# Performance work log

Hardware: AMD Instinct MI355X
Metric: run time of the kernel (lower is better)

## Reference

```python
import jax, jax.numpy as jnp
import numpy as np

K = 4
G = 64
IN_DIM = 256
OUT_DIM = 256
BATCH = 512
T0, T1 = -1.0, 1.0


def setup_inputs() -> dict:
    key = jax.random.key(0)
    kx, kw = jax.random.split(key)
    x = jax.random.uniform(kx, (BATCH, IN_DIM), jnp.float32, T0, T1)
    # xavier_normal_ on [G+K, in, out]: std = sqrt(2 / (fan_in + fan_out)) with fan over last two dims
    std = (2.0 / (IN_DIM + OUT_DIM)) ** 0.5
    w = jax.random.normal(kw, (G + K, IN_DIM, OUT_DIM), jnp.float32) * std
    # knot vector: k-1 repeats of t0, linspace(t0,t1,G+1), k-1 repeats of t1
    t = jnp.concatenate([
        jnp.full((K - 1,), T0, jnp.float32),
        jnp.linspace(T0, T1, G + 1, dtype=jnp.float32),
        jnp.full((K - 1,), T1, jnp.float32),
    ])
    return {"x": x, "w": w, "t": t, "k": K}


def _basis(x, t, k):
    """Cox-de Boor: the k nonzero order-k B-spline basis values at each x.
    Returns (idx, N): idx [..., k] basis indices i-k+1..i, N [..., k] values."""
    n_t = t.shape[0]
    # interval i with t[i] <= x < t[i+1], clipped to the valid span
    i = jnp.clip(jnp.searchsorted(t, x, side='right') - 1, k - 1, n_t - k - 1)
    N = jnp.ones(x.shape + (1,), x.dtype)
    for p in range(1, k):  # static small loop (k=4)
        jj = jnp.arange(1, p + 1)
        left = x[..., None] - t[i[..., None] + 1 - jj]   # [..., p]
        right = t[i[..., None] + jj] - x[..., None]      # [..., p]
        saved = jnp.zeros_like(x)
        vals = []
        for r in range(p):
            d = right[..., r] + left[..., p - 1 - r]      # t[i+r+1] - t[i+r+1-p]
            temp = N[..., r] / d
            vals.append(saved + right[..., r] * temp)
            saved = left[..., p - 1 - r] * temp
        vals.append(saved)
        N = jnp.stack(vals, -1)
    idx = i[..., None] - (k - 1) + jnp.arange(k)
    return idx, N


def reference(x, w, t, k):
    in_dim = x.shape[1]
    n_rows = w.shape[0]
    idx, y1 = _basis(x, t, k)                             # [B,in,k], [B,in,k]
    # last row of w (index -1 == n_rows-1) weights the SiLU residual term
    idx_full = jnp.concatenate(
        [idx, jnp.full(idx.shape[:-1] + (1,), n_rows - 1, idx.dtype)], -1)  # [B,in,k+1]
    silu = x * jax.nn.sigmoid(x)
    y2 = jnp.concatenate([y1, silu[..., None]], -1)       # [B,in,k+1]
    # gather local spline coefficients: w2[b,c,j,o] = w[idx_full[b,c,j], c, o]
    w2 = w[idx_full, jnp.arange(in_dim)[None, :, None], :]  # [B,in,k+1,out]
    return jnp.einsum('bcjo,bcj->bo', w2, y2)             # [B,out]
```

## Files before the change

kernel.cpp:

```cpp
#include <hip/hip_runtime.h>
#include <math.h>
#include <stdint.h>

#define IN_DIM  256
#define OUT_DIM 256
#define NROWS   68
#define NT      71
#define BATCH   512
#define W_ELEMS (NROWS * IN_DIM * OUT_DIM)
#define PART_FLOATS (8 * BATCH * OUT_DIM)

__device__ __forceinline__ uint32_t bf16_rne(float f) {
  uint32_t u = __builtin_bit_cast(uint32_t, f);
  return (u + 0x7fffu + ((u >> 16) & 1u)) >> 16;
}

__global__ __launch_bounds__(256) void cvt_kernel(const float* __restrict__ w,
                                                  uint32_t* __restrict__ wb) {
  const int base = (blockIdx.x * 256 + threadIdx.x) * 8;
  const float4 a = *(const float4*)(w + base);
  const float4 b = *(const float4*)(w + base + 4);
  uint4 o;
  o.x = bf16_rne(a.x) | (bf16_rne(a.y) << 16);
  o.y = bf16_rne(a.z) | (bf16_rne(a.w) << 16);
  o.z = bf16_rne(b.x) | (bf16_rne(b.y) << 16);
  o.w = bf16_rne(b.z) | (bf16_rne(b.w) << 16);
  *(uint4*)(wb + base / 2) = o;
}

__device__ __forceinline__ void fma8(const uint4 q, const float y, float* acc) {
  acc[0] += y * __builtin_bit_cast(float, q.x << 16);
  acc[1] += y * __builtin_bit_cast(float, q.x & 0xffff0000u);
  acc[2] += y * __builtin_bit_cast(float, q.y << 16);
  acc[3] += y * __builtin_bit_cast(float, q.y & 0xffff0000u);
  acc[4] += y * __builtin_bit_cast(float, q.z << 16);
  acc[5] += y * __builtin_bit_cast(float, q.z & 0xffff0000u);
  acc[6] += y * __builtin_bit_cast(float, q.w << 16);
  acc[7] += y * __builtin_bit_cast(float, q.w & 0xffff0000u);
}

__global__ __launch_bounds__(256) void kan_gather_kernel(
    const float* __restrict__ x, const uint4* __restrict__ wp,
    const float* __restrict__ t, float* __restrict__ part) {
  __shared__ float  lt[NT];
  __shared__ float4 nA[32][8];
  __shared__ float  sA[32][8];
  __shared__ int    bA[32][8];
  __shared__ float  red[4][2048];

  const int tid = threadIdx.x;
  const unsigned bid = blockIdx.x;
  const int cchunk = bid & 7;
  const int bgroup = bid >> 3;

  if (tid < NT) lt[tid] = t[tid];
  __syncthreads();

  {
    const int bb = tid >> 5;
    const int cl = tid & 31;
    const float xv = x[(size_t)(bgroup * 8 + bb) * IN_DIM + cchunk * 32 + cl];
    int i = 3 + (int)floorf((xv + 1.0f) * 32.0f);
    i = i < 3 ? 3 : (i > 66 ? 66 : i);
    while (i > 3 && xv < lt[i]) --i;
    while (i < 66 && xv >= lt[i + 1]) ++i;

    float N0 = 1.f, N1 = 0.f, N2 = 0.f, N3 = 0.f;
    {
      const float l1 = xv - lt[i];
      const float r1 = lt[i + 1] - xv;
      const float tp = N0 / (r1 + l1);
      N1 = l1 * tp; N0 = r1 * tp;
    }
    {
      const float l1 = xv - lt[i];
      const float l2 = xv - lt[i - 1];
      const float r1 = lt[i + 1] - xv;
      const float r2 = lt[i + 2] - xv;
      float saved = 0.f;
      const float tp0 = N0 / (r1 + l2);
      const float n0 = saved + r1 * tp0; saved = l2 * tp0;
      const float tp1 = N1 / (r2 + l1);
      const float n1 = saved + r2 * tp1; saved = l1 * tp1;
      N0 = n0; N1 = n1; N2 = saved;
    }
    {
      const float l1 = xv - lt[i];
      const float l2 = xv - lt[i - 1];
      const float l3 = xv - lt[i - 2];
      const float r1 = lt[i + 1] - xv;
      const float r2 = lt[i + 2] - xv;
      const float r3 = lt[i + 3] - xv;
      float saved = 0.f;
      const float tp0 = N0 / (r1 + l3);
      const float n0 = saved + r1 * tp0; saved = l3 * tp0;
      const float tp1 = N1 / (r2 + l2);
      const float n1 = saved + r2 * tp1; saved = l2 * tp1;
      const float tp2 = N2 / (r3 + l1);
      const float n2 = saved + r3 * tp2; saved = l1 * tp2;
      N0 = n0; N1 = n1; N2 = n2; N3 = saved;
    }
    nA[cl][bb] = make_float4(N0, N1, N2, N3);
    sA[cl][bb] = xv / (1.0f + expf(-xv));
    bA[cl][bb] = i - 3;
  }
  __syncthreads();

  const int wv   = tid >> 6;
  const int lane = tid & 63;
  const int half = lane >> 5;
  const int ol   = lane & 31;

  float acc[8][8];
  #pragma unroll
  for (int b = 0; b < 8; ++b) {
    #pragma unroll
    for (int j = 0; j < 8; ++j) acc[b][j] = 0.f;
  }

  for (int pp = 0; pp < 4; ++pp) {
    const int cl = wv * 8 + pp * 2 + half;
    const uint32_t cbase = (uint32_t)((cchunk * 32 + cl) * 32 + ol);
    const uint4 q4 = wp[cbase + 67u * 8192u];
    #pragma unroll
    for (int b = 0; b < 8; ++b) {
      const float4 yv = nA[cl][b];
      const float  ys = sA[cl][b];
      const uint32_t rb = cbase + ((uint32_t)bA[cl][b] << 13);
      const uint4 q0 = wp[rb];
      const uint4 q1 = wp[rb +  8192u];
      const uint4 q2 = wp[rb + 16384u];
      const uint4 q3 = wp[rb + 24576u];
      fma8(q0, yv.x, acc[b]);
      fma8(q1, yv.y, acc[b]);
      fma8(q2, yv.z, acc[b]);
      fma8(q3, yv.w, acc[b]);
      fma8(q4, ys,   acc[b]);
    }
  }

  #pragma unroll
  for (int b = 0; b < 8; ++b) {
    #pragma unroll
    for (int j = 0; j < 8; ++j)
      acc[b][j] += __shfl_xor(acc[b][j], 32, 64);
  }

  if (half == 0) {
    #pragma unroll
    for (int b = 0; b < 8; ++b) {
      #pragma unroll
      for (int j = 0; j < 8; ++j)
        red[wv][b * 256 + ol * 8 + j] = acc[b][j];
    }
  }
  __syncthreads();

  {
    const int b  = tid >> 5;
    const int oo = tid & 31;
    float4 s0 = make_float4(0.f, 0.f, 0.f, 0.f);
    float4 s1 = make_float4(0.f, 0.f, 0.f, 0.f);
    #pragma unroll
    for (int w2 = 0; w2 < 4; ++w2) {
      const float4 a0 = *(const float4*)&red[w2][b * 256 + oo * 8];
      const float4 a1 = *(const float4*)&red[w2][b * 256 + oo * 8 + 4];
      s0.x += a0.x; s0.y += a0.y; s0.z += a0.z; s0.w += a0.w;
      s1.x += a1.x; s1.y += a1.y; s1.z += a1.z; s1.w += a1.w;
    }
    float* dst = part + ((size_t)cchunk * BATCH + bgroup * 8 + b) * OUT_DIM + oo * 8;
    *(float4*)dst       = s0;
    *(float4*)(dst + 4) = s1;
  }
}

__global__ __launch_bounds__(256) void reduce_kernel(const float* __restrict__ part,
                                                     float* __restrict__ out) {
  const int q = blockIdx.x * 256 + threadIdx.x;
  const int S = BATCH * OUT_DIM / 4;
  const float4* p = (const float4*)part;
  float4 s = p[q];
  #pragma unroll
  for (int k = 1; k < 8; ++k) {
    const float4 a = p[q + k * S];
    s.x += a.x; s.y += a.y; s.z += a.z; s.w += a.w;
  }
  ((float4*)out)[q] = s;
}

extern "C" void kernel_launch(void* const* d_in, const int* in_sizes, int n_in,
                              void* d_out, int out_size, void* d_ws, size_t ws_size,
                              hipStream_t stream) {
  const float* x = (const float*)d_in[0];
  const float* w = (const float*)d_in[1];
  const float* t = (const float*)d_in[2];
  float* out  = (float*)d_out;
  float* part = (float*)d_ws;
  uint32_t* wb = (uint32_t*)d_ws + PART_FLOATS;
  cvt_kernel<<<W_ELEMS / (256 * 8), 256, 0, stream>>>(w, wb);
  kan_gather_kernel<<<512, 256, 0, stream>>>(x, (const uint4*)wb, t, part);
  reduce_kernel<<<BATCH * OUT_DIM / 4 / 256, 256, 0, stream>>>(part, out);
}
```

Before: 89.77 us.

## Gather fp32 weights directly and reduce partial sums with atomics

After: 116.2 us. 1.29x slower.

```diff
diff --git a/kernel.cpp b/kernel.cpp
--- a/kernel.cpp
+++ b/kernel.cpp
@@ -7,41 +7,15 @@
 #define NROWS   68
 #define NT      71
 #define BATCH   512
-#define W_ELEMS (NROWS * IN_DIM * OUT_DIM)
-#define PART_FLOATS (8 * BATCH * OUT_DIM)
 
-__device__ __forceinline__ uint32_t bf16_rne(float f) {
-  uint32_t u = __builtin_bit_cast(uint32_t, f);
-  return (u + 0x7fffu + ((u >> 16) & 1u)) >> 16;
+__global__ __launch_bounds__(256) void zero_out_kernel(float* __restrict__ out) {
+  const int q = blockIdx.x * 256 + threadIdx.x;
+  ((float4*)out)[q] = make_float4(0.f, 0.f, 0.f, 0.f);
 }
 
-__global__ __launch_bounds__(256) void cvt_kernel(const float* __restrict__ w,
-                                                  uint32_t* __restrict__ wb) {
-  const int base = (blockIdx.x * 256 + threadIdx.x) * 8;
-  const float4 a = *(const float4*)(w + base);
-  const float4 b = *(const float4*)(w + base + 4);
-  uint4 o;
-  o.x = bf16_rne(a.x) | (bf16_rne(a.y) << 16);
-  o.y = bf16_rne(a.z) | (bf16_rne(a.w) << 16);
-  o.z = bf16_rne(b.x) | (bf16_rne(b.y) << 16);
-  o.w = bf16_rne(b.z) | (bf16_rne(b.w) << 16);
-  *(uint4*)(wb + base / 2) = o;
-}
-
-__device__ __forceinline__ void fma8(const uint4 q, const float y, float* acc) {
-  acc[0] += y * __builtin_bit_cast(float, q.x << 16);
-  acc[1] += y * __builtin_bit_cast(float, q.x & 0xffff0000u);
-  acc[2] += y * __builtin_bit_cast(float, q.y << 16);
-  acc[3] += y * __builtin_bit_cast(float, q.y & 0xffff0000u);
-  acc[4] += y * __builtin_bit_cast(float, q.z << 16);
-  acc[5] += y * __builtin_bit_cast(float, q.z & 0xffff0000u);
-  acc[6] += y * __builtin_bit_cast(float, q.w << 16);
-  acc[7] += y * __builtin_bit_cast(float, q.w & 0xffff0000u);
-}
-
-__global__ __launch_bounds__(256) void kan_gather_kernel(
-    const float* __restrict__ x, const uint4* __restrict__ wp,
-    const float* __restrict__ t, float* __restrict__ part) {
+__global__ __launch_bounds__(256) void kan_gather_fp32_kernel(
+    const float* __restrict__ x, const float* __restrict__ w,
+    const float* __restrict__ t, float* __restrict__ out) {
   __shared__ float  lt[NT];
   __shared__ float4 nA[32][8];
   __shared__ float  sA[32][8];
@@ -108,84 +82,54 @@
 
   const int wv   = tid >> 6;
   const int lane = tid & 63;
-  const int half = lane >> 5;
-  const int ol   = lane & 31;
+  const float4* wf = (const float4*)w;
 
-  float acc[8][8];
+  float acc[8][4];
   #pragma unroll
   for (int b = 0; b < 8; ++b) {
-    #pragma unroll
-    for (int j = 0; j < 8; ++j) acc[b][j] = 0.f;
+    acc[b][0] = 0.f; acc[b][1] = 0.f; acc[b][2] = 0.f; acc[b][3] = 0.f;
   }
 
-  for (int pp = 0; pp < 4; ++pp) {
-    const int cl = wv * 8 + pp * 2 + half;
-    const uint32_t cbase = (uint32_t)((cchunk * 32 + cl) * 32 + ol);
-    const uint4 q4 = wp[cbase + 67u * 8192u];
+  for (int pp = 0; pp < 8; ++pp) {
+    const int cl = wv * 8 + pp;
+    const uint32_t cb = (uint32_t)((cchunk * 32 + cl) * 64 + lane);
+    const float4 q4 = wf[cb + 67u * 16384u];
     #pragma unroll
     for (int b = 0; b < 8; ++b) {
       const float4 yv = nA[cl][b];
       const float  ys = sA[cl][b];
-      const uint32_t rb = cbase + ((uint32_t)bA[cl][b] << 13);
-      const uint4 q0 = wp[rb];
-      const uint4 q1 = wp[rb +  8192u];
-      const uint4 q2 = wp[rb + 16384u];
-      const uint4 q3 = wp[rb + 24576u];
-      fma8(q0, yv.x, acc[b]);
-      fma8(q1, yv.y, acc[b]);
-      fma8(q2, yv.z, acc[b]);
-      fma8(q3, yv.w, acc[b]);
-      fma8(q4, ys,   acc[b]);
+      const uint32_t rb = cb + ((uint32_t)bA[cl][b] * 16384u);
+      const float4 q0 = wf[rb];
+      const float4 q1 = wf[rb + 16384u];
+      const float4 q2 = wf[rb + 32768u];
+      const float4 q3 = wf[rb + 49152u];
+      acc[b][0] += yv.x * q0.x + yv.y * q1.x + yv.z * q2.x + yv.w * q3.x + ys * q4.x;
+      acc[b][1] += yv.x * q0.y + yv.y * q1.y + yv.z * q2.y + yv.w * q3.y + ys * q4.y;
+      acc[b][2] += yv.x * q0.z + yv.y * q1.z + yv.z * q2.z + yv.w * q3.z + ys * q4.z;
+      acc[b][3] += yv.x * q0.w + yv.y * q1.w + yv.z * q2.w + yv.w * q3.w + ys * q4.w;
     }
   }
 
   #pragma unroll
   for (int b = 0; b < 8; ++b) {
-    #pragma unroll
-    for (int j = 0; j < 8; ++j)
-      acc[b][j] += __shfl_xor(acc[b][j], 32, 64);
-  }
-
-  if (half == 0) {
-    #pragma unroll
-    for (int b = 0; b < 8; ++b) {
-      #pragma unroll
-      for (int j = 0; j < 8; ++j)
-        red[wv][b * 256 + ol * 8 + j] = acc[b][j];
-    }
+    float4 v = make_float4(acc[b][0], acc[b][1], acc[b][2], acc[b][3]);
+    *(float4*)&red[wv][b * 256 + lane * 4] = v;
   }
   __syncthreads();
-
   {
     const int b  = tid >> 5;
     const int oo = tid & 31;
-    float4 s0 = make_float4(0.f, 0.f, 0.f, 0.f);
-    float4 s1 = make_float4(0.f, 0.f, 0.f, 0.f);
+    float s[8] = {0.f, 0.f, 0.f, 0.f, 0.f, 0.f, 0.f, 0.f};
     #pragma unroll
     for (int w2 = 0; w2 < 4; ++w2) {
-      const float4 a0 = *(const float4*)&red[w2][b * 256 + oo * 8];
-      const float4 a1 = *(const float4*)&red[w2][b * 256 + oo * 8 + 4];
-      s0.x += a0.x; s0.y += a0.y; s0.z += a0.z; s0.w += a0.w;
-      s1.x += a1.x; s1.y += a1.y; s1.z += a1.z; s1.w += a1.w;
+      const float* rr = &red[w2][b * 256 + oo * 8];
+      #pragma unroll
+      for (int j = 0; j < 8; ++j) s[j] += rr[j];
     }
-    float* dst = part + ((size_t)cchunk * BATCH + bgroup * 8 + b) * OUT_DIM + oo * 8;
-    *(float4*)dst       = s0;
-    *(float4*)(dst + 4) = s1;
+    float* dst = out + ((size_t)(bgroup * 8 + b)) * OUT_DIM + oo * 8;
+    #pragma unroll
+    for (int j = 0; j < 8; ++j) unsafeAtomicAdd(dst + j, s[j]);
   }
-}
-
-__global__ __launch_bounds__(256) void reduce_kernel(const float* __restrict__ part,
-                                                     float* __restrict__ out) {
-  const int q = blockIdx.x * 256 + threadIdx.x;
-  const int S = BATCH * OUT_DIM / 4;
-  const float4* p = (const float4*)part;
-  float4 s = p[q];
-  #pragma unroll
-  for (int k = 1; k < 8; ++k) {
-    const float4 a = p[q + k * S];
-    s.x += a.x; s.y += a.y; s.z += a.z; s.w += a.w;
-  }
-  ((float4*)out)[q] = s;
 }
 
 extern "C" void kernel_launch(void* const* d_in, const int* in_sizes, int n_in,
@@ -194,10 +138,8 @@
   const float* x = (const float*)d_in[0];
   const float* w = (const float*)d_in[1];
   const float* t = (const float*)d_in[2];
-  float* out  = (float*)d_out;
-  float* part = (float*)d_ws;
-  uint32_t* wb = (uint32_t*)d_ws + PART_FLOATS;
-  cvt_kernel<<<W_ELEMS / (256 * 8), 256, 0, stream>>>(w, wb);
-  kan_gather_kernel<<<512, 256, 0, stream>>>(x, (const uint4*)wb, t, part);
-  reduce_kernel<<<BATCH * OUT_DIM / 4 / 256, 256, 0, stream>>>(part, out);
+  float* out = (float*)d_out;
+  (void)d_ws; (void)ws_size;
+  zero_out_kernel<<<BATCH * OUT_DIM / 4 / 256, 256, 0, stream>>>(out);
+  kan_gather_fp32_kernel<<<BATCH / 8 * 8, 256, 0, stream>>>(x, w, t, out);
 }
```

## Halve batch rows per block, double grid, and software-pipeline gather loads

Applied to the files above, without the earlier changes.

New measurement: 97.38 us. +8.5%, slower.

```diff
diff --git a/kernel.cpp b/kernel.cpp
--- a/kernel.cpp
+++ b/kernel.cpp
@@ -39,14 +39,14 @@
   acc[7] += y * __builtin_bit_cast(float, q.w & 0xffff0000u);
 }
 
-__global__ __launch_bounds__(256) void kan_gather_kernel(
+__global__ __launch_bounds__(256, 4) void kan_gather_kernel(
     const float* __restrict__ x, const uint4* __restrict__ wp,
     const float* __restrict__ t, float* __restrict__ part) {
   __shared__ float  lt[NT];
-  __shared__ float4 nA[32][8];
-  __shared__ float  sA[32][8];
-  __shared__ int    bA[32][8];
-  __shared__ float  red[4][2048];
+  __shared__ float4 nA[32][4];
+  __shared__ float  sA[32][4];
+  __shared__ int    bA[32][4];
+  __shared__ float  red[4][1024];
 
   const int tid = threadIdx.x;
   const unsigned bid = blockIdx.x;
@@ -56,10 +56,10 @@
   if (tid < NT) lt[tid] = t[tid];
   __syncthreads();
 
-  {
+  if (tid < 128) {
     const int bb = tid >> 5;
     const int cl = tid & 31;
-    const float xv = x[(size_t)(bgroup * 8 + bb) * IN_DIM + cchunk * 32 + cl];
+    const float xv = x[(size_t)(bgroup * 4 + bb) * IN_DIM + cchunk * 32 + cl];
     int i = 3 + (int)floorf((xv + 1.0f) * 32.0f);
     i = i < 3 ? 3 : (i > 66 ? 66 : i);
     while (i > 3 && xv < lt[i]) --i;
@@ -111,66 +111,72 @@
   const int half = lane >> 5;
   const int ol   = lane & 31;
 
-  float acc[8][8];
+  float acc[4][8];
   #pragma unroll
-  for (int b = 0; b < 8; ++b) {
+  for (int b = 0; b < 4; ++b) {
     #pragma unroll
     for (int j = 0; j < 8; ++j) acc[b][j] = 0.f;
   }
 
   for (int pp = 0; pp < 4; ++pp) {
     const int cl = wv * 8 + pp * 2 + half;
-    const uint32_t cbase = (uint32_t)((cchunk * 32 + cl) * 32 + ol);
-    const uint4 q4 = wp[cbase + 67u * 8192u];
-    #pragma unroll
-    for (int b = 0; b < 8; ++b) {
-      const float4 yv = nA[cl][b];
-      const float  ys = sA[cl][b];
-      const uint32_t rb = cbase + ((uint32_t)bA[cl][b] << 13);
-      const uint4 q0 = wp[rb];
-      const uint4 q1 = wp[rb +  8192u];
-      const uint4 q2 = wp[rb + 16384u];
-      const uint4 q3 = wp[rb + 24576u];
-      fma8(q0, yv.x, acc[b]);
-      fma8(q1, yv.y, acc[b]);
-      fma8(q2, yv.z, acc[b]);
-      fma8(q3, yv.w, acc[b]);
-      fma8(q4, ys,   acc[b]);
-    }
+    const uint32_t cb = (uint32_t)((cchunk * 32 + cl) * 32 + ol);
+    const uint4 q4 = wp[cb + 67u * 8192u];
+
+    const int r0 = bA[cl][0], r1 = bA[cl][1], r2 = bA[cl][2], r3 = bA[cl][3];
+    const float4 y0 = nA[cl][0], y1 = nA[cl][1], y2 = nA[cl][2], y3 = nA[cl][3];
+    const float  s0 = sA[cl][0], s1 = sA[cl][1], s2 = sA[cl][2], s3 = sA[cl][3];
+
+#define LD(P0, P1, P2, P3, RB)                                          \
+    { const uint32_t rb = cb + (uint32_t)(RB) * 8192u;                  \
+      P0 = wp[rb]; P1 = wp[rb +  8192u];                                \
+      P2 = wp[rb + 16384u]; P3 = wp[rb + 24576u]; }
+#define FM(P0, P1, P2, P3, YV, YS, bb)                                  \
+    { fma8(P0, YV.x, acc[bb]); fma8(P1, YV.y, acc[bb]);                 \
+      fma8(P2, YV.z, acc[bb]); fma8(P3, YV.w, acc[bb]);                 \
+      fma8(q4, YS,   acc[bb]); }
+
+    uint4 A0, A1, A2, A3, B0, B1, B2, B3;
+    LD(A0, A1, A2, A3, r0)
+    LD(B0, B1, B2, B3, r1)
+    FM(A0, A1, A2, A3, y0, s0, 0)
+    LD(A0, A1, A2, A3, r2)
+    FM(B0, B1, B2, B3, y1, s1, 1)
+    LD(B0, B1, B2, B3, r3)
+    FM(A0, A1, A2, A3, y2, s2, 2)
+    FM(B0, B1, B2, B3, y3, s3, 3)
+#undef LD
+#undef FM
   }
 
   #pragma unroll
-  for (int b = 0; b < 8; ++b) {
+  for (int b = 0; b < 4; ++b) {
     #pragma unroll
     for (int j = 0; j < 8; ++j)
-      acc[b][j] += __shfl_xor(acc[b][j], 32, 64);
-  }
-
+      acc[b][j] += __shfl_xor(acc[b][j], 32);
+  }
   if (half == 0) {
     #pragma unroll
-    for (int b = 0; b < 8; ++b) {
-      #pragma unroll
-      for (int j = 0; j < 8; ++j)
-        red[wv][b * 256 + ol * 8 + j] = acc[b][j];
+    for (int b = 0; b < 4; ++b) {
+      *(float4*)&red[wv][b * 256 + ol * 8]     = make_float4(acc[b][0], acc[b][1], acc[b][2], acc[b][3]);
+      *(float4*)&red[wv][b * 256 + ol * 8 + 4] = make_float4(acc[b][4], acc[b][5], acc[b][6], acc[b][7]);
     }
   }
   __syncthreads();
 
   {
-    const int b  = tid >> 5;
-    const int oo = tid & 31;
-    float4 s0 = make_float4(0.f, 0.f, 0.f, 0.f);
-    float4 s1 = make_float4(0.f, 0.f, 0.f, 0.f);
-    #pragma unroll
-    for (int w2 = 0; w2 < 4; ++w2) {
-      const float4 a0 = *(const float4*)&red[w2][b * 256 + oo * 8];
-      const float4 a1 = *(const float4*)&red[w2][b * 256 + oo * 8 + 4];
-      s0.x += a0.x; s0.y += a0.y; s0.z += a0.z; s0.w += a0.w;
-      s1.x += a1.x; s1.y += a1.y; s1.z += a1.z; s1.w += a1.w;
-    }
-    float* dst = part + ((size_t)cchunk * BATCH + bgroup * 8 + b) * OUT_DIM + oo * 8;
-    *(float4*)dst       = s0;
-    *(float4*)(dst + 4) = s1;
+    const int b  = tid >> 6;
+    const int o4 = tid & 63;
+    const float4 a0 = *(const float4*)&red[0][b * 256 + o4 * 4];
+    const float4 a1 = *(const float4*)&red[1][b * 256 + o4 * 4];
+    const float4 a2 = *(const float4*)&red[2][b * 256 + o4 * 4];
+    const float4 a3 = *(const float4*)&red[3][b * 256 + o4 * 4];
+    float4 s;
+    s.x = (a0.x + a1.x) + (a2.x + a3.x);
+    s.y = (a0.y + a1.y) + (a2.y + a3.y);
+    s.z = (a0.z + a1.z) + (a2.z + a3.z);
+    s.w = (a0.w + a1.w) + (a2.w + a3.w);
+    *(float4*)(part + ((size_t)cchunk * BATCH + bgroup * 4 + b) * OUT_DIM + o4 * 4) = s;
   }
 }
 
@@ -198,6 +204,6 @@
   float* part = (float*)d_ws;
   uint32_t* wb = (uint32_t*)d_ws + PART_FLOATS;
   cvt_kernel<<<W_ELEMS / (256 * 8), 256, 0, stream>>>(w, wb);
-  kan_gather_kernel<<<512, 256, 0, stream>>>(x, (const uint4*)wb, t, part);
+  kan_gather_kernel<<<1024, 256, 0, stream>>>(x, (const uint4*)wb, t, part);
   reduce_kernel<<<BATCH * OUT_DIM / 4 / 256, 256, 0, stream>>>(part, out);
 }
```
